# Optimization experiments

Hardware: AMD Instinct MI355X
Metric: run time of the kernel (lower is better)

## Reference

```python
import jax, jax.numpy as jnp
import numpy as np
import math

EPS = 1e-5

def conv1x1(x, w):
    # x: (B,C,H,W), w: (O,C)
    return jnp.einsum('bchw,oc->bohw', x, w)

def bn(x, gamma, beta, mean, var):
    # inference-mode batchnorm, params shape (C,)
    s = (gamma / jnp.sqrt(var + EPS))[None, :, None, None]
    b = (beta - mean * gamma / jnp.sqrt(var + EPS))[None, :, None, None]
    return x * s + b

def setup_inputs() -> dict:
    key = jax.random.key(0)
    ks = jax.random.split(key, 16)
    B, C1, C2, OUT, W, H = 4, 256, 64, 64, 64, 64
    inp = {
        'rgb': jax.random.normal(ks[0], (B, C2, W, H), jnp.float32),
        'dep': jax.random.normal(ks[1], (B, C1, W, H), jnp.float32),
        # dep fusion conv (1x1) + BN
        'conv_w': jax.random.normal(ks[2], (C2, C1), jnp.float32) * (1.0 / np.sqrt(C1)),
        'bn1_g': jax.random.uniform(ks[3], (C2,), jnp.float32, 0.5, 1.5),
        'bn1_b': jax.random.normal(ks[4], (C2,), jnp.float32) * 0.1,
        'bn1_m': jax.random.normal(ks[5], (C2,), jnp.float32) * 0.1,
        'bn1_v': jax.random.uniform(ks[6], (C2,), jnp.float32, 0.5, 1.5),
        # attention projections (1x1, no bias)
        'rgb_w': jax.random.normal(ks[7], (C2, C2), jnp.float32) * (1.0 / np.sqrt(C2)),
        'dep_w': jax.random.normal(ks[8], (C2, C2), jnp.float32) * (1.0 / np.sqrt(C2)),
        # mlp: ConvBNReLU(C2,24,1) then ConvBNSig(24,OUT,1)
        'mlp1_w': jax.random.normal(ks[9], (24, C2), jnp.float32) * (1.0 / np.sqrt(C2)),
        'bn2_g': jax.random.uniform(ks[10], (24,), jnp.float32, 0.5, 1.5),
        'bn2_b': jax.random.normal(ks[11], (24,), jnp.float32) * 0.1,
        'bn2_m': jax.random.normal(ks[12], (24,), jnp.float32) * 0.1,
        'bn2_v': jax.random.uniform(ks[13], (24,), jnp.float32, 0.5, 1.5),
        'mlp2_w': jax.random.normal(ks[14], (OUT, 24), jnp.float32) * (1.0 / np.sqrt(24)),
        'bn3_g': jax.random.uniform(jax.random.fold_in(key, 20), (OUT,), jnp.float32, 0.5, 1.5),
        'bn3_b': jax.random.normal(jax.random.fold_in(key, 21), (OUT,), jnp.float32) * 0.1,
        'bn3_m': jax.random.normal(jax.random.fold_in(key, 22), (OUT,), jnp.float32) * 0.1,
        'bn3_v': jax.random.uniform(jax.random.fold_in(key, 23), (OUT,), jnp.float32, 0.5, 1.5),
    }
    return inp

def reference(rgb, dep, conv_w, bn1_g, bn1_b, bn1_m, bn1_v, rgb_w, dep_w,
              mlp1_w, bn2_g, bn2_b, bn2_m, bn2_v, mlp2_w, bn3_g, bn3_b, bn3_m, bn3_v):
    # dep = ConvBNReLU(dep)
    dep = jax.nn.relu(bn(conv1x1(dep, conv_w), bn1_g, bn1_b, bn1_m, bn1_v))
    rgbd = rgb + dep
    B, C, W, H = rgb.shape
    N = W * H
    proj_rgb = conv1x1(rgb, rgb_w).reshape(B, C, N)  # (B,C,N)
    proj_dep = conv1x1(dep, dep_w).reshape(B, C, N)  # (B,C,N)
    # energy[b,i,j] = <proj_rgb[:,i], proj_dep[:,j]> / sqrt(C)
    energy = jnp.einsum('bci,bcj->bij', proj_rgb, proj_dep) / math.sqrt(C)
    attn = jax.nn.softmax(energy, axis=1)  # torch Softmax(dim=1): over rows i
    att_r = jnp.einsum('bci,bij->bcj', proj_rgb, attn)
    att_b = jnp.einsum('bci,bij->bcj', proj_dep, attn)
    output = (att_r + att_b).reshape(B, C, W, H) + rgbd
    gap = output.mean(axis=(2, 3), keepdims=True)  # (B,C,1,1)
    h = jax.nn.relu(bn(conv1x1(gap, mlp1_w), bn2_g, bn2_b, bn2_m, bn2_v))
    gate = jax.nn.sigmoid(bn(conv1x1(h, mlp2_w), bn3_g, bn3_b, bn3_m, bn3_v))
    return gate
```

## Files before the change

kernel.cpp:

```cpp
#include <hip/hip_runtime.h>
#include <hip/hip_bf16.h>


typedef __bf16 bf16;
typedef __bf16 bf16x4 __attribute__((ext_vector_type(4)));
typedef __bf16 bf16x8 __attribute__((ext_vector_type(8)));
typedef float  f32x4  __attribute__((ext_vector_type(4)));
typedef float  float4v __attribute__((ext_vector_type(4)));
typedef short  s4     __attribute__((ext_vector_type(4)));

#define MFMA_BF16(a, b, c) __builtin_amdgcn_mfma_f32_16x16x32_bf16((a), (b), (c), 0, 0, 0)

#if defined(__has_builtin)
# if __has_builtin(__builtin_amdgcn_mfma_f32_16x16x16bf16_1k)
#  define MFMA16_BUILTIN(a, b, c) __builtin_amdgcn_mfma_f32_16x16x16bf16_1k((a), (b), (c), 0, 0, 0)
# elif __has_builtin(__builtin_amdgcn_mfma_f32_16x16x16_bf16)
#  define MFMA16_BUILTIN(a, b, c) __builtin_amdgcn_mfma_f32_16x16x16_bf16((a), (b), (c), 0, 0, 0)
# endif
#endif

__device__ __forceinline__ f32x4 MFMA16(s4 a, s4 b, f32x4 c) {
#ifdef MFMA16_BUILTIN
    return MFMA16_BUILTIN(a, b, c);
#else
    asm("v_mfma_f32_16x16x16_bf16 %0, %1, %2, %0" : "+v"(c) : "v"(a), "v"(b));
    return c;
#endif
}

#if defined(__has_builtin)
# if __has_builtin(__builtin_amdgcn_exp2f)
#  define EXP2(x) __builtin_amdgcn_exp2f(x)
# else
#  define EXP2(x) exp2f(x)
# endif
#else
# define EXP2(x) exp2f(x)
#endif

#define K_E 0.18033688f

__device__ __forceinline__ int swz128(int row, int colByte) {
    return row * 128 + (colByte ^ ((row & 7) << 4));
}
__device__ __forceinline__ int swz512(int row, int colByte) {
    return row * 512 + (colByte ^ ((row & 15) << 4));
}

__global__ __launch_bounds__(256) void k_prep(
    const float* __restrict__ conv_w, const float* __restrict__ rgb_w,
    const float* __restrict__ dep_w,
    bf16* __restrict__ wC, bf16* __restrict__ wR, bf16* __restrict__ wD)
{
    const int gid = blockIdx.x * 256 + threadIdx.x;
    bf16x8 v;
    if (gid < 2048) {
        const int t = gid >> 9, kk = (gid >> 6) & 7, lane = gid & 63;
        const float* src = conv_w + (size_t)(t * 16 + (lane & 15)) * 256
                                  + kk * 32 + (lane >> 4) * 8;
        #pragma unroll
        for (int j = 0; j < 8; ++j) v[j] = (bf16)src[j];
        *(bf16x8*)(wC + (size_t)gid * 8) = v;
    } else if (gid < 2560) {
        const int g = gid - 2048;
        const int t = g >> 7, kk = (g >> 6) & 1, lane = g & 63;
        const float* src = rgb_w + (size_t)(t * 16 + (lane & 15)) * 64
                                 + kk * 32 + (lane >> 4) * 8;
        #pragma unroll
        for (int j = 0; j < 8; ++j) v[j] = (bf16)src[j];
        *(bf16x8*)(wR + (size_t)g * 8) = v;
    } else {
        const int g = gid - 2560;
        const int t = g >> 7, kk = (g >> 6) & 1, lane = g & 63;
        const float* src = dep_w + (size_t)(t * 16 + (lane & 15)) * 64
                                 + kk * 32 + (lane >> 4) * 8;
        #pragma unroll
        for (int j = 0; j < 8; ++j) v[j] = (bf16)src[j];
        *(bf16x8*)(wD + (size_t)g * 8) = v;
    }
}

__global__ __launch_bounds__(512, 2) void k_front(
    const float* __restrict__ rgb, const float* __restrict__ dep,
    const bf16* __restrict__ wC, const bf16* __restrict__ wR,
    const bf16* __restrict__ wD,
    const float* __restrict__ bn1_g, const float* __restrict__ bn1_b,
    const float* __restrict__ bn1_m, const float* __restrict__ bn1_v,
    bf16* __restrict__ prF, bf16* __restrict__ pdF, bf16* __restrict__ pvF,
    float* __restrict__ rgbdPart)
{
    const int bid = blockIdx.x;
    const int xcd = bid & 7;
    const int b    = xcd >> 1;
    const int tile = ((bid >> 3) << 1) | (xcd & 1);
    const int p0   = tile * 32;
    const int tid = threadIdx.x;
    const int w   = tid >> 6;
    const int lane = tid & 63;
    const int l15 = lane & 15;
    const int lg  = lane >> 4;
    const int ot4 = w & 3;
    const int ot  = ot4 * 16;
    const int ph  = w >> 2;

    __shared__ float s1[64], b1[64];
    __shared__ __align__(16) unsigned char ldsC[32 * 512];
    __shared__ __align__(16) unsigned char ldsR[32 * 128];
    __shared__ __align__(16) unsigned char ldsD[32 * 128];
    __shared__ float red[8][64];

    const float* depb = dep + (size_t)b * 256 * 4096;
    const float* rgbb = rgb + (size_t)b * 64 * 4096;

    {
        const int c0 = tid >> 3, seg = tid & 7;
        #pragma unroll
        for (int r = 0; r < 4; ++r) {
            const int c = r * 64 + c0;
            float4v v = *(const float4v*)(depb + (size_t)c * 4096 + p0 + seg * 4);
            #pragma unroll
            for (int k = 0; k < 4; ++k)
                *(bf16*)(ldsC + swz512(seg * 4 + k, c * 2)) = (bf16)v[k];
        }
        float4v v = *(const float4v*)(rgbb + (size_t)c0 * 4096 + p0 + seg * 4);
        #pragma unroll
        for (int k = 0; k < 4; ++k)
            *(bf16*)(ldsR + swz128(seg * 4 + k, c0 * 2)) = (bf16)v[k];
        if (tid < 64) {
            float sc = bn1_g[tid] * rsqrtf(bn1_v[tid] + 1e-5f);
            s1[tid] = sc;
            b1[tid] = bn1_b[tid] - bn1_m[tid] * sc;
        }
    }
    __syncthreads();

    const int prow = ph * 16 + l15;
    bf16x8 aW[8];
    #pragma unroll
    for (int kk = 0; kk < 8; ++kk)
        aW[kk] = *(const bf16x8*)(wC + ((size_t)(ot4 * 8 + kk) * 64 + lane) * 8);
    f32x4 acc = {0.f, 0.f, 0.f, 0.f};
    #pragma unroll
    for (int kk = 0; kk < 8; ++kk) {
        bf16x8 bF = *(const bf16x8*)(ldsC + swz512(prow, (kk * 32 + lg * 8) * 2));
        acc = MFMA_BF16(aW[kk], bF, acc);
    }
    {
        const int o0 = ot + lg * 4;
        bf16x4 v4;
        #pragma unroll
        for (int r = 0; r < 4; ++r) {
            float x = acc[r] * s1[o0 + r] + b1[o0 + r];
            v4[r] = (bf16)(x > 0.f ? x : 0.f);
        }
        *(bf16x4*)(ldsD + swz128(prow, o0 * 2)) = v4;
    }
    __syncthreads();

    bf16x8 aR[2], aD[2];
    #pragma unroll
    for (int kk = 0; kk < 2; ++kk) {
        aR[kk] = *(const bf16x8*)(wR + ((size_t)(ot4 * 2 + kk) * 64 + lane) * 8);
        aD[kk] = *(const bf16x8*)(wD + ((size_t)(ot4 * 2 + kk) * 64 + lane) * 8);
    }
    f32x4 accR = {0.f, 0.f, 0.f, 0.f}, accD = {0.f, 0.f, 0.f, 0.f};
    #pragma unroll
    for (int kk = 0; kk < 2; ++kk) {
        const int cb = (kk * 32 + lg * 8) * 2;
        bf16x8 bR = *(const bf16x8*)(ldsR + swz128(prow, cb));
        bf16x8 bD = *(const bf16x8*)(ldsD + swz128(prow, cb));
        accR = MFMA_BF16(aR[kk], bR, accR);
        accD = MFMA_BF16(aD[kk], bD, accD);
    }
    {
        const int o0 = ot + lg * 4;
        const size_t itile = (size_t)tile * 2 + ph;
        const size_t fbase = (size_t)b * 262144 + itile * 1024;
        const size_t prOff = fbase + (size_t)(o0 >> 3) * 128 + l15 * 8 + (o0 & 7);
        bf16x4 vR, vD;
        #pragma unroll
        for (int r = 0; r < 4; ++r) {
            vR[r] = (bf16)(accR[r] * K_E);
            vD[r] = (bf16)accD[r];
        }
        *(bf16x4*)(prF + prOff) = vR;
        *(bf16x4*)(pdF + prOff) = vD;
        const size_t pvBase = fbase + ot4 * 256 + (l15 >> 2) * 64 + lg * 16 + (l15 & 3);
        #pragma unroll
        for (int r = 0; r < 4; ++r)
            pvF[pvBase + r * 4] = (bf16)(accR[r] + accD[r]);
    }

    {
        const int c = tid & 63, g8 = tid >> 6;
        float sum = 0.f;
        #pragma unroll
        for (int q = 0; q < 4; ++q) {
            const int pp = g8 * 4 + q;
            sum += (float)*(const bf16*)(ldsR + swz128(pp, c * 2))
                 + (float)*(const bf16*)(ldsD + swz128(pp, c * 2));
        }
        red[g8][c] = sum;
    }
    __syncthreads();
    if (tid < 64) {
        float s = 0.f;
        #pragma unroll
        for (int g = 0; g < 8; ++g) s += red[g][tid];
        rgbdPart[((size_t)b * 128 + tile) * 64 + tid] = s;
    }
}

__global__ __launch_bounds__(512, 2) void k_col(
    const bf16* __restrict__ prF, const bf16* __restrict__ pdF,
    const bf16* __restrict__ pvF, float* __restrict__ gapPart)
{
    const int bid = blockIdx.x;
    const int xcd = bid & 7, b = xcd >> 1;
    const int jt64 = ((bid >> 3) << 1) | (xcd & 1);
    const int tid = threadIdx.x;
    const int ih = tid >> 6, lane = tid & 63;
    const int l15 = lane & 15, lg = lane >> 4;

    __shared__ float zred[8][64];
    __shared__ float zfull[64];
    __shared__ float gred[8][64];

    const bf16* prb = prF + (size_t)b * 262144;
    const bf16* pdb = pdF + (size_t)b * 262144;
    const bf16* pvb = pvF + (size_t)b * 262144;

    bf16x8 B0[4], B1[4];
    #pragma unroll
    for (int jt = 0; jt < 4; ++jt) {
        const bf16* q = pdb + (size_t)(jt64 * 4 + jt) * 1024 + lane * 8;
        B0[jt] = *(const bf16x8*)q;
        B1[jt] = *(const bf16x8*)(q + 512);
    }

    f32x4 acc[4][4];
    #pragma unroll
    for (int jt = 0; jt < 4; ++jt)
        #pragma unroll
        for (int cb = 0; cb < 4; ++cb)
            acc[jt][cb] = (f32x4){0.f, 0.f, 0.f, 0.f};
    float z[4] = {0.f, 0.f, 0.f, 0.f};

    const bf16* pA = prb + (size_t)ih * 32 * 1024;
    const bf16* pV = pvb + (size_t)ih * 32 * 1024;

    bf16x8 a0 = *(const bf16x8*)(pA + lane * 8);
    bf16x8 a1 = *(const bf16x8*)(pA + 512 + lane * 8);
    bf16x4 v0 = *(const bf16x4*)(pV + lane * 4);
    bf16x4 v1 = *(const bf16x4*)(pV + 256 + lane * 4);
    bf16x4 v2 = *(const bf16x4*)(pV + 512 + lane * 4);
    bf16x4 v3 = *(const bf16x4*)(pV + 768 + lane * 4);

    for (int t = 0; t < 32; ++t) {
        const bf16x8 ca0 = a0, ca1 = a1;
        const bf16x4 cv0 = v0, cv1 = v1, cv2 = v2, cv3 = v3;
        if (t < 31) {
            pA += 1024; pV += 1024;
            a0 = *(const bf16x8*)(pA + lane * 8);
            a1 = *(const bf16x8*)(pA + 512 + lane * 8);
            v0 = *(const bf16x4*)(pV + lane * 4);
            v1 = *(const bf16x4*)(pV + 256 + lane * 4);
            v2 = *(const bf16x4*)(pV + 512 + lane * 4);
            v3 = *(const bf16x4*)(pV + 768 + lane * 4);
        }
        #pragma unroll
        for (int jt = 0; jt < 4; ++jt) {
            f32x4 e = {0.f, 0.f, 0.f, 0.f};
            e = MFMA_BF16(ca0, B0[jt], e);
            e = MFMA_BF16(ca1, B1[jt], e);
            bf16x4 ph;
            #pragma unroll
            for (int r = 0; r < 4; ++r) {
                float pf = EXP2(e[r]);
                z[jt] += pf;
                ph[r] = (bf16)pf;
            }
            const s4 pB = __builtin_bit_cast(s4, ph);
            acc[jt][0] = MFMA16(__builtin_bit_cast(s4, cv0), pB, acc[jt][0]);
            acc[jt][1] = MFMA16(__builtin_bit_cast(s4, cv1), pB, acc[jt][1]);
            acc[jt][2] = MFMA16(__builtin_bit_cast(s4, cv2), pB, acc[jt][2]);
            acc[jt][3] = MFMA16(__builtin_bit_cast(s4, cv3), pB, acc[jt][3]);
        }
    }

    #pragma unroll
    for (int jt = 0; jt < 4; ++jt) {
        float zv = z[jt];
        zv += __shfl_xor(zv, 16);
        zv += __shfl_xor(zv, 32);
        if (lane < 16) zred[ih][jt * 16 + lane] = zv;
    }
    __syncthreads();
    if (tid < 64) {
        float s = 0.f;
        #pragma unroll
        for (int k = 0; k < 8; ++k) s += zred[k][tid];
        zfull[tid] = s;
    }
    __syncthreads();

    float zinv[4];
    #pragma unroll
    for (int jt = 0; jt < 4; ++jt) {
        const float zj = zfull[jt * 16 + l15];
        float zi = __builtin_amdgcn_rcpf(zj);
        zinv[jt] = zi * (2.0f - zj * zi);
    }
    #pragma unroll
    for (int cb = 0; cb < 4; ++cb) {
        #pragma unroll
        for (int r = 0; r < 4; ++r) {
            float v = acc[0][cb][r] * zinv[0] + acc[1][cb][r] * zinv[1]
                    + acc[2][cb][r] * zinv[2] + acc[3][cb][r] * zinv[3];
            v += __shfl_xor(v, 1);
            v += __shfl_xor(v, 2);
            v += __shfl_xor(v, 4);
            v += __shfl_xor(v, 8);
            if (l15 == 0) gred[ih][cb * 16 + lg * 4 + r] = v;
        }
    }
    __syncthreads();
    if (tid < 64) {
        float s = 0.f;
        #pragma unroll
        for (int k = 0; k < 8; ++k) s += gred[k][tid];
        gapPart[((size_t)b * 64 + jt64) * 64 + tid] = s;
    }
}

__global__ __launch_bounds__(256) void k_gate(
    const float* __restrict__ gapPart, const float* __restrict__ rgbdPart,
    const float* __restrict__ mlp1_w,
    const float* __restrict__ bn2_g, const float* __restrict__ bn2_b,
    const float* __restrict__ bn2_m, const float* __restrict__ bn2_v,
    const float* __restrict__ mlp2_w,
    const float* __restrict__ bn3_g, const float* __restrict__ bn3_b,
    const float* __restrict__ bn3_m, const float* __restrict__ bn3_v,
    float* __restrict__ out)
{
    const int b = blockIdx.x, tid = threadIdx.x;
    const int c = tid & 63, g = tid >> 6;
    __shared__ float red[4][64];
    __shared__ float gv[64], h[24];

    float acc = 0.f;
    const float* rp = rgbdPart + ((size_t)b * 128 + g * 32) * 64 + c;
    #pragma unroll 4
    for (int t = 0; t < 32; ++t) acc += rp[t * 64];
    const float* gp = gapPart + ((size_t)b * 64 + g * 16) * 64 + c;
    #pragma unroll 4
    for (int t = 0; t < 16; ++t) acc += gp[t * 64];
    red[g][c] = acc;
    __syncthreads();
    if (tid < 64)
        gv[tid] = ((red[0][tid] + red[1][tid]) + (red[2][tid] + red[3][tid]))
                  * (1.f / 4096.f);
    __syncthreads();
    if (tid < 24) {
        float a = 0.f;
        #pragma unroll
        for (int cc = 0; cc < 64; ++cc) a += mlp1_w[tid * 64 + cc] * gv[cc];
        float sc = bn2_g[tid] * rsqrtf(bn2_v[tid] + 1e-5f);
        a = a * sc + bn2_b[tid] - bn2_m[tid] * sc;
        h[tid] = a > 0.f ? a : 0.f;
    }
    __syncthreads();
    if (tid < 64) {
        float u = 0.f;
        #pragma unroll
        for (int o = 0; o < 24; ++o) u += mlp2_w[tid * 24 + o] * h[o];
        float sc = bn3_g[tid] * rsqrtf(bn3_v[tid] + 1e-5f);
        u = u * sc + bn3_b[tid] - bn3_m[tid] * sc;
        out[b * 64 + tid] = 1.f / (1.f + __expf(-u));
    }
}

extern "C" void kernel_launch(void* const* d_in, const int* in_sizes, int n_in,
                              void* d_out, int out_size, void* d_ws, size_t ws_size,
                              hipStream_t stream)
{
    const float* rgb    = (const float*)d_in[0];
    const float* dep    = (const float*)d_in[1];
    const float* conv_w = (const float*)d_in[2];
    const float* bn1_g  = (const float*)d_in[3];
    const float* bn1_b  = (const float*)d_in[4];
    const float* bn1_m  = (const float*)d_in[5];
    const float* bn1_v  = (const float*)d_in[6];
    const float* rgb_w  = (const float*)d_in[7];
    const float* dep_w  = (const float*)d_in[8];
    const float* mlp1_w = (const float*)d_in[9];
    const float* bn2_g  = (const float*)d_in[10];
    const float* bn2_b  = (const float*)d_in[11];
    const float* bn2_m  = (const float*)d_in[12];
    const float* bn2_v  = (const float*)d_in[13];
    const float* mlp2_w = (const float*)d_in[14];
    const float* bn3_g  = (const float*)d_in[15];
    const float* bn3_b  = (const float*)d_in[16];
    const float* bn3_m  = (const float*)d_in[17];
    const float* bn3_v  = (const float*)d_in[18];

    char* ws = (char*)d_ws;
    bf16*  prF      = (bf16*)(ws);
    bf16*  pdF      = (bf16*)(ws + (2u << 20));
    bf16*  pvF      = (bf16*)(ws + (4u << 20));
    float* rgbdPart = (float*)(ws + (6u << 20));
    float* gapPart  = (float*)(ws + (6u << 20) + (128u << 10));
    bf16*  wC       = (bf16*)(ws + (6u << 20) + (192u << 10));
    bf16*  wR       = (bf16*)(ws + (6u << 20) + (224u << 10));
    bf16*  wD       = (bf16*)(ws + (6u << 20) + (232u << 10));

    k_prep<<<12, 256, 0, stream>>>(conv_w, rgb_w, dep_w, wC, wR, wD);
    k_front<<<512, 512, 0, stream>>>(rgb, dep, wC, wR, wD,
                                     bn1_g, bn1_b, bn1_m, bn1_v,
                                     prF, pdF, pvF, rgbdPart);
    k_col<<<256, 512, 0, stream>>>(prF, pdF, pvF, gapPart);
    k_gate<<<4, 256, 0, stream>>>(gapPart, rgbdPart, mlp1_w,
                                  bn2_g, bn2_b, bn2_m, bn2_v, mlp2_w,
                                  bn3_g, bn3_b, bn3_m, bn3_v, (float*)d_out);
}
```

Baseline: 48.34 us.

## Fold weight prep into front kernel and gate MLP into column kernel

Removes the separate weight-conversion kernel: each front block now loads the fp32 conv, rgb and dep weights, converts them to bf16 into swizzled LDS, and reads its MFMA operands from there. Removes the separate gate kernel: column blocks bump a global atomic counter after writing their partial GAP sums, and the last finisher reduces all partials and runs the tiny MLP plus sigmoid for all four batches. This is meant to cut two kernel launches and their inter-kernel gaps. In exchange every front block re-reads about 64KB of weights from cache and uses more LDS, and the last-block pattern depends on a counter that is reset inside the front kernel plus thread fences.

Result: slower. 51.95 us (+7.5%).

```diff
diff --git a/kernel.cpp b/kernel.cpp
--- a/kernel.cpp
+++ b/kernel.cpp
@@ -47,47 +47,25 @@
     return row * 512 + (colByte ^ ((row & 15) << 4));
 }
 
-__global__ __launch_bounds__(256) void k_prep(
-    const float* __restrict__ conv_w, const float* __restrict__ rgb_w,
-    const float* __restrict__ dep_w,
-    bf16* __restrict__ wC, bf16* __restrict__ wR, bf16* __restrict__ wD)
-{
-    const int gid = blockIdx.x * 256 + threadIdx.x;
-    bf16x8 v;
-    if (gid < 2048) {
-        const int t = gid >> 9, kk = (gid >> 6) & 7, lane = gid & 63;
-        const float* src = conv_w + (size_t)(t * 16 + (lane & 15)) * 256
-                                  + kk * 32 + (lane >> 4) * 8;
-        #pragma unroll
-        for (int j = 0; j < 8; ++j) v[j] = (bf16)src[j];
-        *(bf16x8*)(wC + (size_t)gid * 8) = v;
-    } else if (gid < 2560) {
-        const int g = gid - 2048;
-        const int t = g >> 7, kk = (g >> 6) & 1, lane = g & 63;
-        const float* src = rgb_w + (size_t)(t * 16 + (lane & 15)) * 64
-                                 + kk * 32 + (lane >> 4) * 8;
-        #pragma unroll
-        for (int j = 0; j < 8; ++j) v[j] = (bf16)src[j];
-        *(bf16x8*)(wR + (size_t)g * 8) = v;
-    } else {
-        const int g = gid - 2560;
-        const int t = g >> 7, kk = (g >> 6) & 1, lane = g & 63;
-        const float* src = dep_w + (size_t)(t * 16 + (lane & 15)) * 64
-                                 + kk * 32 + (lane >> 4) * 8;
-        #pragma unroll
-        for (int j = 0; j < 8; ++j) v[j] = (bf16)src[j];
-        *(bf16x8*)(wD + (size_t)g * 8) = v;
-    }
-}
+#define OW_W   0
+#define OW_WR  32768
+#define OW_WD  40960
+#define OT_C   0
+#define OT_R   16384
+#define OT_D   20480
+#define O_S1   49152
+#define O_B1   49408
+#define O_RED  49664
+#define SMEMA  51712
 
 __global__ __launch_bounds__(512, 2) void k_front(
     const float* __restrict__ rgb, const float* __restrict__ dep,
-    const bf16* __restrict__ wC, const bf16* __restrict__ wR,
-    const bf16* __restrict__ wD,
+    const float* __restrict__ conv_w,
     const float* __restrict__ bn1_g, const float* __restrict__ bn1_b,
     const float* __restrict__ bn1_m, const float* __restrict__ bn1_v,
+    const float* __restrict__ rgb_w, const float* __restrict__ dep_w,
     bf16* __restrict__ prF, bf16* __restrict__ pdF, bf16* __restrict__ pvF,
-    float* __restrict__ rgbdPart)
+    float* __restrict__ rgbdPart, int* __restrict__ counter)
 {
     const int bid = blockIdx.x;
     const int xcd = bid & 7;
@@ -103,29 +81,41 @@
     const int ot  = ot4 * 16;
     const int ph  = w >> 2;
 
-    __shared__ float s1[64], b1[64];
-    __shared__ __align__(16) unsigned char ldsC[32 * 512];
-    __shared__ __align__(16) unsigned char ldsR[32 * 128];
-    __shared__ __align__(16) unsigned char ldsD[32 * 128];
-    __shared__ float red[8][64];
-
-    const float* depb = dep + (size_t)b * 256 * 4096;
-    const float* rgbb = rgb + (size_t)b * 64 * 4096;
-
-    {
-        const int c0 = tid >> 3, seg = tid & 7;
-        #pragma unroll
-        for (int r = 0; r < 4; ++r) {
-            const int c = r * 64 + c0;
-            float4v v = *(const float4v*)(depb + (size_t)c * 4096 + p0 + seg * 4);
-            #pragma unroll
-            for (int k = 0; k < 4; ++k)
-                *(bf16*)(ldsC + swz512(seg * 4 + k, c * 2)) = (bf16)v[k];
-        }
-        float4v v = *(const float4v*)(rgbb + (size_t)c0 * 4096 + p0 + seg * 4);
-        #pragma unroll
-        for (int k = 0; k < 4; ++k)
-            *(bf16*)(ldsR + swz128(seg * 4 + k, c0 * 2)) = (bf16)v[k];
+    if (bid == 0 && tid == 0) *counter = 0;
+
+    __shared__ __align__(16) unsigned char smem[SMEMA];
+    float* s1 = (float*)(smem + O_S1);
+    float* b1 = (float*)(smem + O_B1);
+    float* red = (float*)(smem + O_RED);
+
+    {
+        unsigned char* ldsW  = smem + OW_W;
+        unsigned char* ldsWR = smem + OW_WR;
+        unsigned char* ldsWD = smem + OW_WD;
+        #pragma unroll
+        for (int q = 0; q < 8; ++q) {
+            const int idx = (q * 512 + tid) * 4;
+            float4v v = *(const float4v*)(conv_w + idx);
+            const int o = idx >> 8, c = idx & 255;
+            bf16x4 h;
+            #pragma unroll
+            for (int j = 0; j < 4; ++j) h[j] = (bf16)v[j];
+            *(bf16x4*)(ldsW + swz512(o, c * 2)) = h;
+        }
+        #pragma unroll
+        for (int q = 0; q < 2; ++q) {
+            const int idx = (q * 512 + tid) * 4;
+            const int o = idx >> 6, c = idx & 63;
+            float4v v = *(const float4v*)(rgb_w + idx);
+            bf16x4 h;
+            #pragma unroll
+            for (int j = 0; j < 4; ++j) h[j] = (bf16)v[j];
+            *(bf16x4*)(ldsWR + swz128(o, c * 2)) = h;
+            v = *(const float4v*)(dep_w + idx);
+            #pragma unroll
+            for (int j = 0; j < 4; ++j) h[j] = (bf16)v[j];
+            *(bf16x4*)(ldsWD + swz128(o, c * 2)) = h;
+        }
         if (tid < 64) {
             float sc = bn1_g[tid] * rsqrtf(bn1_v[tid] + 1e-5f);
             s1[tid] = sc;
@@ -134,11 +124,46 @@
     }
     __syncthreads();
 
+    bf16x8 aW[8], aR[2], aD[2];
+    {
+        const unsigned char* ldsW  = smem + OW_W;
+        const unsigned char* ldsWR = smem + OW_WR;
+        const unsigned char* ldsWD = smem + OW_WD;
+        const int row = ot + l15;
+        #pragma unroll
+        for (int kk = 0; kk < 8; ++kk)
+            aW[kk] = *(const bf16x8*)(ldsW + swz512(row, (kk * 32 + lg * 8) * 2));
+        #pragma unroll
+        for (int kk = 0; kk < 2; ++kk) {
+            aR[kk] = *(const bf16x8*)(ldsWR + swz128(row, (kk * 32 + lg * 8) * 2));
+            aD[kk] = *(const bf16x8*)(ldsWD + swz128(row, (kk * 32 + lg * 8) * 2));
+        }
+    }
+    __syncthreads();
+
+    unsigned char* ldsC = smem + OT_C;
+    unsigned char* ldsR = smem + OT_R;
+    unsigned char* ldsD = smem + OT_D;
+    const float* depb = dep + (size_t)b * 256 * 4096;
+    const float* rgbb = rgb + (size_t)b * 64 * 4096;
+    {
+        const int c0 = tid >> 3, seg = tid & 7;
+        #pragma unroll
+        for (int r = 0; r < 4; ++r) {
+            const int c = r * 64 + c0;
+            float4v v = *(const float4v*)(depb + (size_t)c * 4096 + p0 + seg * 4);
+            #pragma unroll
+            for (int k = 0; k < 4; ++k)
+                *(bf16*)(ldsC + swz512(seg * 4 + k, c * 2)) = (bf16)v[k];
+        }
+        float4v v = *(const float4v*)(rgbb + (size_t)c0 * 4096 + p0 + seg * 4);
+        #pragma unroll
+        for (int k = 0; k < 4; ++k)
+            *(bf16*)(ldsR + swz128(seg * 4 + k, c0 * 2)) = (bf16)v[k];
+    }
+    __syncthreads();
+
     const int prow = ph * 16 + l15;
-    bf16x8 aW[8];
-    #pragma unroll
-    for (int kk = 0; kk < 8; ++kk)
-        aW[kk] = *(const bf16x8*)(wC + ((size_t)(ot4 * 8 + kk) * 64 + lane) * 8);
     f32x4 acc = {0.f, 0.f, 0.f, 0.f};
     #pragma unroll
     for (int kk = 0; kk < 8; ++kk) {
@@ -157,12 +182,6 @@
     }
     __syncthreads();
 
-    bf16x8 aR[2], aD[2];
-    #pragma unroll
-    for (int kk = 0; kk < 2; ++kk) {
-        aR[kk] = *(const bf16x8*)(wR + ((size_t)(ot4 * 2 + kk) * 64 + lane) * 8);
-        aD[kk] = *(const bf16x8*)(wD + ((size_t)(ot4 * 2 + kk) * 64 + lane) * 8);
-    }
     f32x4 accR = {0.f, 0.f, 0.f, 0.f}, accD = {0.f, 0.f, 0.f, 0.f};
     #pragma unroll
     for (int kk = 0; kk < 2; ++kk) {
@@ -200,20 +219,29 @@
             sum += (float)*(const bf16*)(ldsR + swz128(pp, c * 2))
                  + (float)*(const bf16*)(ldsD + swz128(pp, c * 2));
         }
-        red[g8][c] = sum;
+        red[g8 * 64 + c] = sum;
     }
     __syncthreads();
     if (tid < 64) {
         float s = 0.f;
         #pragma unroll
-        for (int g = 0; g < 8; ++g) s += red[g][tid];
+        for (int g = 0; g < 8; ++g) s += red[g * 64 + tid];
         rgbdPart[((size_t)b * 128 + tile) * 64 + tid] = s;
     }
 }
 
 __global__ __launch_bounds__(512, 2) void k_col(
     const bf16* __restrict__ prF, const bf16* __restrict__ pdF,
-    const bf16* __restrict__ pvF, float* __restrict__ gapPart)
+    const bf16* __restrict__ pvF,
+    float* __restrict__ gapPart, const float* __restrict__ rgbdPart,
+    int* __restrict__ counter,
+    const float* __restrict__ mlp1_w,
+    const float* __restrict__ bn2_g, const float* __restrict__ bn2_b,
+    const float* __restrict__ bn2_m, const float* __restrict__ bn2_v,
+    const float* __restrict__ mlp2_w,
+    const float* __restrict__ bn3_g, const float* __restrict__ bn3_b,
+    const float* __restrict__ bn3_m, const float* __restrict__ bn3_v,
+    float* __restrict__ out)
 {
     const int bid = blockIdx.x;
     const int xcd = bid & 7, b = xcd >> 1;
@@ -225,6 +253,10 @@
     __shared__ float zred[8][64];
     __shared__ float zfull[64];
     __shared__ float gred[8][64];
+    __shared__ float gv4[4][64];
+    __shared__ float h4[4][24];
+    __shared__ int winflag;
+    if (tid == 0) winflag = 0;
 
     const bf16* prb = prF + (size_t)b * 262144;
     const bf16* pdb = pdF + (size_t)b * 262144;
@@ -330,53 +362,48 @@
         #pragma unroll
         for (int k = 0; k < 8; ++k) s += gred[k][tid];
         gapPart[((size_t)b * 64 + jt64) * 64 + tid] = s;
-    }
-}
-
-__global__ __launch_bounds__(256) void k_gate(
-    const float* __restrict__ gapPart, const float* __restrict__ rgbdPart,
-    const float* __restrict__ mlp1_w,
-    const float* __restrict__ bn2_g, const float* __restrict__ bn2_b,
-    const float* __restrict__ bn2_m, const float* __restrict__ bn2_v,
-    const float* __restrict__ mlp2_w,
-    const float* __restrict__ bn3_g, const float* __restrict__ bn3_b,
-    const float* __restrict__ bn3_m, const float* __restrict__ bn3_v,
-    float* __restrict__ out)
-{
-    const int b = blockIdx.x, tid = threadIdx.x;
-    const int c = tid & 63, g = tid >> 6;
-    __shared__ float red[4][64];
-    __shared__ float gv[64], h[24];
-
-    float acc = 0.f;
-    const float* rp = rgbdPart + ((size_t)b * 128 + g * 32) * 64 + c;
-    #pragma unroll 4
-    for (int t = 0; t < 32; ++t) acc += rp[t * 64];
-    const float* gp = gapPart + ((size_t)b * 64 + g * 16) * 64 + c;
-    #pragma unroll 4
-    for (int t = 0; t < 16; ++t) acc += gp[t * 64];
-    red[g][c] = acc;
-    __syncthreads();
-    if (tid < 64)
-        gv[tid] = ((red[0][tid] + red[1][tid]) + (red[2][tid] + red[3][tid]))
-                  * (1.f / 4096.f);
-    __syncthreads();
-    if (tid < 24) {
-        float a = 0.f;
-        #pragma unroll
-        for (int cc = 0; cc < 64; ++cc) a += mlp1_w[tid * 64 + cc] * gv[cc];
-        float sc = bn2_g[tid] * rsqrtf(bn2_v[tid] + 1e-5f);
-        a = a * sc + bn2_b[tid] - bn2_m[tid] * sc;
-        h[tid] = a > 0.f ? a : 0.f;
-    }
-    __syncthreads();
-    if (tid < 64) {
-        float u = 0.f;
-        #pragma unroll
-        for (int o = 0; o < 24; ++o) u += mlp2_w[tid * 24 + o] * h[o];
-        float sc = bn3_g[tid] * rsqrtf(bn3_v[tid] + 1e-5f);
-        u = u * sc + bn3_b[tid] - bn3_m[tid] * sc;
-        out[b * 64 + tid] = 1.f / (1.f + __expf(-u));
+        __threadfence();
+        int old = atomicAdd(counter, 1);
+        if (old == 256 * 64 - 1) winflag = 1;
+    }
+    __syncthreads();
+
+    if (winflag) {
+        __threadfence();
+        const int wb = ih >> 1, half = ih & 1;
+        float acc2 = 0.f;
+        const float* gp = gapPart + ((size_t)wb * 64 + half * 32) * 64 + lane;
+        #pragma unroll 4
+        for (int r = 0; r < 32; ++r) acc2 += gp[r * 64];
+        const float* rp = rgbdPart + ((size_t)wb * 128 + half * 64) * 64 + lane;
+        #pragma unroll 4
+        for (int r = 0; r < 64; ++r) acc2 += rp[r * 64];
+        gred[ih][lane] = acc2;
+        __syncthreads();
+        if (tid < 256) {
+            const int b4 = tid >> 6, c = tid & 63;
+            gv4[b4][c] = (gred[2 * b4][c] + gred[2 * b4 + 1][c]) * (1.f / 4096.f);
+        }
+        __syncthreads();
+        if (tid < 96) {
+            const int b4 = tid / 24, o = tid % 24;
+            float a = 0.f;
+            #pragma unroll
+            for (int cc = 0; cc < 64; ++cc) a += mlp1_w[o * 64 + cc] * gv4[b4][cc];
+            float sc = bn2_g[o] * rsqrtf(bn2_v[o] + 1e-5f);
+            a = a * sc + bn2_b[o] - bn2_m[o] * sc;
+            h4[b4][o] = a > 0.f ? a : 0.f;
+        }
+        __syncthreads();
+        if (tid < 256) {
+            const int b4 = tid >> 6, c = tid & 63;
+            float u = 0.f;
+            #pragma unroll
+            for (int o = 0; o < 24; ++o) u += mlp2_w[c * 24 + o] * h4[b4][o];
+            float sc = bn3_g[c] * rsqrtf(bn3_v[c] + 1e-5f);
+            u = u * sc + bn3_b[c] - bn3_m[c] * sc;
+            out[b4 * 64 + c] = 1.f / (1.f + __expf(-u));
+        }
     }
 }
 
@@ -410,16 +437,14 @@
     bf16*  pvF      = (bf16*)(ws + (4u << 20));
     float* rgbdPart = (float*)(ws + (6u << 20));
     float* gapPart  = (float*)(ws + (6u << 20) + (128u << 10));
-    bf16*  wC       = (bf16*)(ws + (6u << 20) + (192u << 10));
-    bf16*  wR       = (bf16*)(ws + (6u << 20) + (224u << 10));
-    bf16*  wD       = (bf16*)(ws + (6u << 20) + (232u << 10));
-
-    k_prep<<<12, 256, 0, stream>>>(conv_w, rgb_w, dep_w, wC, wR, wD);
-    k_front<<<512, 512, 0, stream>>>(rgb, dep, wC, wR, wD,
+    int*   counter  = (int*)  (ws + (6u << 20) + (192u << 10));
+
+    k_front<<<512, 512, 0, stream>>>(rgb, dep, conv_w,
                                      bn1_g, bn1_b, bn1_m, bn1_v,
-                                     prF, pdF, pvF, rgbdPart);
-    k_col<<<256, 512, 0, stream>>>(prF, pdF, pvF, gapPart);
-    k_gate<<<4, 256, 0, stream>>>(gapPart, rgbdPart, mlp1_w,
-                                  bn2_g, bn2_b, bn2_m, bn2_v, mlp2_w,
-                                  bn3_g, bn3_b, bn3_m, bn3_v, (float*)d_out);
-}
+                                     rgb_w, dep_w,
+                                     prF, pdF, pvF, rgbdPart, counter);
+    k_col<<<256, 512, 0, stream>>>(prF, pdF, pvF, gapPart, rgbdPart, counter,
+                                   mlp1_w, bn2_g, bn2_b, bn2_m, bn2_v,
+                                   mlp2_w, bn3_g, bn3_b, bn3_m, bn3_v,
+                                   (float*)d_out);
+}
```
